# Kernel optimization log

Hardware: AMD Instinct MI355X
Metric: run time of the kernel (lower is better)

The kernel has to match this reference:

```python
import jax, jax.numpy as jnp
import numpy as np
from jax import lax

STRIDE, PAD, K = 1, 1, 3


def conv2d(x, w, b, stride, pad):
    y = lax.conv_general_dilated(x, w, (stride, stride), [(pad, pad), (pad, pad)],
                                 dimension_numbers=('NCHW', 'OIHW', 'NCHW'))
    return y + b[None, :, None, None]


def deform_conv2d(x, offset, mask, weight, stride, pad):
    # torchvision DeformConv2d v2 (modulated): offset channels are (dy, dx) pairs per tap.
    B, C, H, W = x.shape
    O = weight.shape[0]
    K2 = K * K
    Ho = (H + 2 * pad - K) // stride + 1
    Wo = (W + 2 * pad - K) // stride + 1
    off = offset.reshape(B, K2, 2, Ho, Wo)
    dy, dx = off[:, :, 0], off[:, :, 1]                      # [B,K2,Ho,Wo]
    ki = (jnp.arange(K2) // K).astype(x.dtype)[None, :, None, None]
    kj = (jnp.arange(K2) % K).astype(x.dtype)[None, :, None, None]
    hg = (jnp.arange(Ho) * stride - pad).astype(x.dtype)[None, None, :, None]
    wg = (jnp.arange(Wo) * stride - pad).astype(x.dtype)[None, None, None, :]
    py = hg + ki + dy                                        # sampling y coord [B,K2,Ho,Wo]
    px = wg + kj + dx
    y0 = jnp.floor(py)
    x0 = jnp.floor(px)
    ly = py - y0
    lx = px - x0
    y0i = y0.astype(jnp.int32)
    x0i = x0.astype(jnp.int32)
    x_flat = x.reshape(B, C, H * W)

    def gather(iy, ix):
        valid = ((iy >= 0) & (iy < H) & (ix >= 0) & (ix < W)).astype(x.dtype)
        idx = jnp.clip(iy, 0, H - 1) * W + jnp.clip(ix, 0, W - 1)   # [B,K2,Ho,Wo]
        v = jax.vmap(lambda xf, id_: xf[:, id_])(x_flat, idx)       # [B,C,K2,Ho,Wo]
        return v * valid[:, None]

    v = ((1 - ly) * (1 - lx))[:, None] * gather(y0i, x0i) \
      + ((1 - ly) * lx)[:, None] * gather(y0i, x0i + 1) \
      + (ly * (1 - lx))[:, None] * gather(y0i + 1, x0i) \
      + (ly * lx)[:, None] * gather(y0i + 1, x0i + 1)
    v = v * mask[:, None]                                    # modulate per tap
    return jnp.einsum('bckhw,ock->bohw', v, weight.reshape(O, C, K2))


def setup_inputs():
    key = jax.random.key(0)
    ks = jax.random.split(key, 5)
    B, C, H, W, O = 4, 64, 96, 96, 128
    x = jax.random.normal(ks[0], (B, C, H, W), jnp.float32)
    offset_w = jax.random.normal(ks[1], (2 * K * K, C, K, K), jnp.float32) * 0.01
    offset_b = jax.random.normal(ks[2], (2 * K * K,), jnp.float32) * 0.1
    mod_w = jax.random.normal(ks[3], (K * K, C, K, K), jnp.float32) * 0.01
    mod_b = jnp.zeros((K * K,), jnp.float32)
    deform_w = jax.random.normal(ks[4], (O, C, K, K), jnp.float32) * (1.0 / np.sqrt(C * K * K))
    return {"x": x, "offset_w": offset_w, "offset_b": offset_b,
            "mod_w": mod_w, "mod_b": mod_b, "deform_w": deform_w}


def reference(x, offset_w, offset_b, mod_w, mod_b, deform_w):
    offset = conv2d(x, offset_w, offset_b, STRIDE, PAD)
    modulator = 2.0 * jax.nn.sigmoid(conv2d(x, mod_w, mod_b, STRIDE, PAD))
    return deform_conv2d(x, offset, modulator, deform_w, STRIDE, PAD)
```

## Files before the change

kernel.cpp:

```cpp
#include <hip/hip_runtime.h>
#include <math.h>

#define Bc 4
#define Cc 64
#define Hh 96
#define Ww 96
#define Oo 128
#define HW 9216
#define PT 32
#define NPB 288
#define RR 7
#define RC 38
#define RS 72

typedef __attribute__((ext_vector_type(8))) short bf16x8;
typedef __attribute__((ext_vector_type(4))) float f32x4;
typedef __attribute__((ext_vector_type(4))) unsigned int u32x4;

__device__ inline float bf_lo(unsigned u) {
    return __builtin_bit_cast(float, u << 16);
}
__device__ inline float bf_hi(unsigned u) {
    return __builtin_bit_cast(float, u & 0xFFFF0000u);
}
__device__ inline unsigned cvt_pk_bf16(float lo, float hi) {
    unsigned r;
    asm("v_cvt_pk_bf16_f32 %0, %1, %2" : "=v"(r) : "v"(lo), "v"(hi));
    return r;
}

__global__ __launch_bounds__(256) void k_pre(
    const float* __restrict__ dw, const float* __restrict__ ow,
    const float* __restrict__ mw, const float* __restrict__ x,
    unsigned short* __restrict__ wTmF, unsigned short* __restrict__ w27F,
    unsigned short* __restrict__ xT)
{
    const int bid = blockIdx.x;
    const int t = threadIdx.x;
    if (bid < 180) {
        int i2 = (bid * 256 + t) * 2;
        if (i2 < 9 * 8 * 2 * 512) {
            int j = i2 & 7;
            int l = (i2 >> 3) & 63, fb = i2 >> 9;
            int s = fb & 1, m = (fb >> 1) & 7, k = fb >> 4;
            int oc = m * 16 + (l & 15);
            int c = s * 32 + (l >> 4) * 8 + j;
            float f0 = dw[(oc * 64 + c) * 9 + k];
            float f1 = dw[(oc * 64 + c + 1) * 9 + k];
            *(unsigned*)(wTmF + i2) = cvt_pk_bf16(f0, f1);
        } else {
            int jj = i2 - 9 * 8 * 2 * 512;
            if (jj < 9 * 2 * 2 * 512) {
                int j = jj & 7, l = (jj >> 3) & 63, fb2 = jj >> 9;
                int nt = fb2 & 1, s = (fb2 >> 1) & 1, k = fb2 >> 2;
                int ch = nt * 16 + (l & 15);
                int c = s * 32 + (l >> 4) * 8 + j;
                float f0 = 0.f, f1 = 0.f;
                if (ch < 18) {
                    f0 = ow[(ch * 64 + c) * 9 + k];
                    f1 = ow[(ch * 64 + c + 1) * 9 + k];
                } else if (ch < 27) {
                    f0 = mw[((ch - 18) * 64 + c) * 9 + k];
                    f1 = mw[((ch - 18) * 64 + c + 1) * 9 + k];
                }
                *(unsigned*)(w27F + jj) = cvt_pk_bf16(f0, f1);
            }
        }
    } else {
        int gp = (bid - 180) * 256 + t;
        int b = gp / HW;
        int p = gp - b * HW;
        const float* xb = x + (size_t)b * Cc * HW + p;
        unsigned short* op = xT + (size_t)gp * 64;
#pragma unroll
        for (int q = 0; q < 8; ++q) {
            union { bf16x8 v8; unsigned u[4]; } u;
#pragma unroll
            for (int c = 0; c < 8; c += 2) {
                float f0 = xb[(size_t)(q * 8 + c) * HW];
                float f1 = xb[(size_t)(q * 8 + c + 1) * HW];
                u.u[c >> 1] = cvt_pk_bf16(f0, f1);
            }
            *(bf16x8*)(op + q * 8) = u.v8;
        }
    }
}

template <int K0, int K1>
__device__ __forceinline__ void sample_gemm(
    const short (&reg)[RR * RC * RS],
    const unsigned short* __restrict__ xTb,
    const unsigned short* __restrict__ wb,
    const float (&pw)[9][4][PT], const int (&pi)[9][4][PT],
    int pos_l, int cq, f32x4 (&acc)[8])
{
#pragma unroll
    for (int kk = K0; kk < K1; ++kk) {
        const float w0 = pw[kk][0][pos_l], w1 = pw[kk][1][pos_l];
        const float w2 = pw[kk][2][pos_l], w3 = pw[kk][3][pos_l];
        const int i0 = pi[kk][0][pos_l], i1 = pi[kk][1][pos_l];
        const int i2 = pi[kk][2][pos_l], i3 = pi[kk][3][pos_l];
        const unsigned long long anybad = __ballot((i0 | i1 | i2 | i3) < 0);

#pragma unroll
        for (int s = 0; s < 2; ++s) {
            const int so = s * 32 + cq;
            bf16x8 c0, c1, c2, c3;
            if (anybad == 0) {
                c0 = *(const bf16x8*)(&reg[i0 + so]);
                c1 = *(const bf16x8*)(&reg[i1 + so]);
                c2 = *(const bf16x8*)(&reg[i2 + so]);
                c3 = *(const bf16x8*)(&reg[i3 + so]);
            } else {
                c0 = (i0 < 0) ? *(const bf16x8*)(xTb + (i0 & 0x7FFFFFFF) + so)
                              : *(const bf16x8*)(&reg[i0 + so]);
                c1 = (i1 < 0) ? *(const bf16x8*)(xTb + (i1 & 0x7FFFFFFF) + so)
                              : *(const bf16x8*)(&reg[i1 + so]);
                c2 = (i2 < 0) ? *(const bf16x8*)(xTb + (i2 & 0x7FFFFFFF) + so)
                              : *(const bf16x8*)(&reg[i2 + so]);
                c3 = (i3 < 0) ? *(const bf16x8*)(xTb + (i3 & 0x7FFFFFFF) + so)
                              : *(const bf16x8*)(&reg[i3 + so]);
            }
            const u32x4 U0 = __builtin_bit_cast(u32x4, c0);
            const u32x4 U1 = __builtin_bit_cast(u32x4, c1);
            const u32x4 U2 = __builtin_bit_cast(u32x4, c2);
            const u32x4 U3 = __builtin_bit_cast(u32x4, c3);
            union { bf16x8 v8; unsigned u[4]; } B;
#pragma unroll
            for (int p = 0; p < 4; ++p) {
                float r0 = w0 * bf_lo(U0[p]) + w1 * bf_lo(U1[p])
                         + w2 * bf_lo(U2[p]) + w3 * bf_lo(U3[p]);
                float r1 = w0 * bf_hi(U0[p]) + w1 * bf_hi(U1[p])
                         + w2 * bf_hi(U2[p]) + w3 * bf_hi(U3[p]);
                B.u[p] = cvt_pk_bf16(r0, r1);
            }
#pragma unroll
            for (int m = 0; m < 8; ++m) {
                bf16x8 A = *(const bf16x8*)(wb + (size_t)((kk * 16 + m * 2 + s) << 9));
                acc[m] = __builtin_amdgcn_mfma_f32_16x16x32_bf16(A, B.v8, acc[m], 0, 0, 0);
            }
        }
    }
}

__global__ __launch_bounds__(256, 3) void k_fused(
    const unsigned short* __restrict__ xT, const float* __restrict__ ob,
    const float* __restrict__ mb, const unsigned short* __restrict__ w27F,
    const unsigned short* __restrict__ wTmF, float* __restrict__ out)
{
    __shared__ union RU {
        short reg[RR * RC * RS];
        float mg[8 * 520];
    } R;
    __shared__ float s_pw[9][4][PT];
    __shared__ int   s_pi[9][4][PT];
    __shared__ float offm_s[27 * 33];

    const int t = threadIdx.x;
    const int lid = (blockIdx.x & 7) * 144 + (blockIdx.x >> 3);
    const int bb = lid / NPB;
    const int tile = lid - bb * NPB;
    const int ho = tile / 3;
    const int wo0 = (tile - ho * 3) * 32;
    const int wv = t >> 6;
    const int l = t & 63;
    const int lr = l & 15;
    const int quad = l >> 4;

    const unsigned short* xTb = xT + (size_t)bb * HW * 64;

    static const bf16x8 zero8 = {0, 0, 0, 0, 0, 0, 0, 0};
    for (int i = t; i < RR * RC * 8; i += 256) {
        int q = i & 7;
        int rcx = i >> 3;
        int col = rcx % RC, r = rcx / RC;
        int h = ho - 3 + r, w = wo0 - 3 + col;
        bf16x8 val = zero8;
        if ((unsigned)h < (unsigned)Hh && (unsigned)w < (unsigned)Ww)
            val = *(const bf16x8*)(xTb + ((size_t)(h * Ww + w)) * 64 + q * 8);
        *(bf16x8*)&R.reg[(r * RC + col) * RS + q * 8] = val;
    }
    __syncthreads();

    {
        f32x4 acc_o = {0.f, 0.f, 0.f, 0.f};
        const int mt1 = wv & 1;
        const int nt1 = wv >> 1;
#pragma unroll
        for (int k9 = 0; k9 < 9; ++k9) {
            const int di = k9 / 3, dj = k9 % 3;
            const short* ar =
                &R.reg[((di + 2) * RC + mt1 * 16 + lr + dj + 2) * RS + quad * 8];
#pragma unroll
            for (int s = 0; s < 2; ++s) {
                bf16x8 a = *(const bf16x8*)(ar + s * 32);
                bf16x8 b = *(const bf16x8*)(w27F + (((k9 * 2 + s) * 2 + nt1) << 9) + l * 8);
                acc_o = __builtin_amdgcn_mfma_f32_16x16x32_bf16(a, b, acc_o, 0, 0, 0);
            }
        }
        int ch = nt1 * 16 + lr;
        if (ch < 27) {
#pragma unroll
            for (int r = 0; r < 4; ++r)
                offm_s[ch * 33 + mt1 * 16 + quad * 4 + r] = acc_o[r];
        }
    }
    __syncthreads();

    for (int i = t; i < 27 * PT; i += 256) {
        int ch = i >> 5, pos = i & 31;
        float v = offm_s[ch * 33 + pos];
        if (ch < 18) v += ob[ch];
        else         v = 2.f / (1.f + expf(-(v + mb[ch - 18])));
        offm_s[ch * 33 + pos] = v;
    }
    __syncthreads();
    for (int i = t; i < 9 * PT; i += 256) {
        int kk = i >> 5, pos = i & 31;
        float dy = offm_s[(2 * kk) * 33 + pos];
        float dx = offm_s[(2 * kk + 1) * 33 + pos];
        float mm = offm_s[(18 + kk) * 33 + pos];
        float py = (float)(ho - 1 + kk / 3) + dy;
        float px = (float)(wo0 + pos - 1 + kk % 3) + dx;
        float fy = floorf(py), fx = floorf(px);
        float ly = py - fy, lx = px - fx;
        int y0 = (int)fy, x0 = (int)fx;
        int y1 = y0 + 1, x1 = x0 + 1;
        float v00 = ((unsigned)y0 < (unsigned)Hh && (unsigned)x0 < (unsigned)Ww) ? 1.f : 0.f;
        float v01 = ((unsigned)y0 < (unsigned)Hh && (unsigned)x1 < (unsigned)Ww) ? 1.f : 0.f;
        float v10 = ((unsigned)y1 < (unsigned)Hh && (unsigned)x0 < (unsigned)Ww) ? 1.f : 0.f;
        float v11 = ((unsigned)y1 < (unsigned)Hh && (unsigned)x1 < (unsigned)Ww) ? 1.f : 0.f;
        s_pw[kk][0][pos] = (1.f - ly) * (1.f - lx) * mm * v00;
        s_pw[kk][1][pos] = (1.f - ly) * lx * mm * v01;
        s_pw[kk][2][pos] = ly * (1.f - lx) * mm * v10;
        s_pw[kk][3][pos] = ly * lx * mm * v11;

        auto mkidx = [&](float valid, int y, int xx) -> int {
            if (valid == 0.f) return 0;
            int ry = y - (ho - 3), rx = xx - (wo0 - 3);
            if ((unsigned)ry < (unsigned)RR && (unsigned)rx < (unsigned)RC)
                return (ry * RC + rx) * RS;
            return (int)(0x80000000u | (unsigned)((y * Ww + xx) * 64));
        };
        s_pi[kk][0][pos] = mkidx(v00, y0, x0);
        s_pi[kk][1][pos] = mkidx(v01, y0, x1);
        s_pi[kk][2][pos] = mkidx(v10, y1, x0);
        s_pi[kk][3][pos] = mkidx(v11, y1, x1);
    }
    __syncthreads();

    const int nt = wv & 1;
    const int tg = wv >> 1;
    const int pos_l = nt * 16 + lr;
    const int cq = quad * 8;

    f32x4 acc[8];
#pragma unroll
    for (int m = 0; m < 8; ++m) acc[m] = (f32x4){0.f, 0.f, 0.f, 0.f};

    const unsigned short* wb = wTmF + l * 8;

    if (tg == 0)
        sample_gemm<0, 5>(R.reg, xTb, wb, s_pw, s_pi, pos_l, cq, acc);
    else
        sample_gemm<5, 9>(R.reg, xTb, wb, s_pw, s_pi, pos_l, cq, acc);

    __syncthreads();
    if (tg == 1) {
#pragma unroll
        for (int m = 0; m < 8; ++m)
            *(f32x4*)&R.mg[m * 520 + (nt * 64 + l) * 4] = acc[m];
    }
    __syncthreads();
    if (tg == 0) {
        float* outp = out + (size_t)bb * Oo * HW + tile * PT + nt * 16 + lr;
#pragma unroll
        for (int m = 0; m < 8; ++m) {
            f32x4 o = acc[m] + *(const f32x4*)&R.mg[m * 520 + (nt * 64 + l) * 4];
#pragma unroll
            for (int r = 0; r < 4; ++r) {
                int oc = m * 16 + quad * 4 + r;
                outp[(size_t)oc * HW] = o[r];
            }
        }
    }
}

extern "C" void kernel_launch(void* const* d_in, const int* in_sizes, int n_in,
                              void* d_out, int out_size, void* d_ws, size_t ws_size,
                              hipStream_t stream) {
    const float* x  = (const float*)d_in[0];
    const float* ow = (const float*)d_in[1];
    const float* ob = (const float*)d_in[2];
    const float* mw = (const float*)d_in[3];
    const float* mb = (const float*)d_in[4];
    const float* dw = (const float*)d_in[5];
    float* out = (float*)d_out;

    unsigned short* wTmF = (unsigned short*)d_ws;
    unsigned short* w27F = wTmF + 9 * 8 * 2 * 512;
    unsigned short* xT   = w27F + 9 * 2 * 2 * 512;

    hipLaunchKernelGGL(k_pre, dim3(324), dim3(256), 0, stream,
                       dw, ow, mw, x, wTmF, w27F, xT);
    hipLaunchKernelGGL(k_fused, dim3(Bc * NPB), dim3(256), 0, stream,
                       xT, ob, mb, w27F, wTmF, out);
}
```

Baseline: 108.2 us.

## Split deform sampling taps across eight waves with LDS tree reduction

Doubles the fused kernel block to 512 threads so four wave-groups each take 2-3 of the 9 kernel taps instead of two groups taking 4-5. Partial MFMA accumulators are combined through a two-stage LDS reduction before the output store. This shortens each wave's serial sampling and MFMA chain and raises wave count per CU. In exchange it adds extra barriers and LDS traffic, leaves half the waves idle in the offset conv, and drops full unrolling of the tap loop because the bounds are now runtime values.

```diff
diff --git a/kernel.cpp b/kernel.cpp
--- a/kernel.cpp
+++ b/kernel.cpp
@@ -86,16 +86,14 @@
     }
 }
 
-template <int K0, int K1>
 __device__ __forceinline__ void sample_gemm(
     const short (&reg)[RR * RC * RS],
     const unsigned short* __restrict__ xTb,
     const unsigned short* __restrict__ wb,
     const float (&pw)[9][4][PT], const int (&pi)[9][4][PT],
-    int pos_l, int cq, f32x4 (&acc)[8])
+    int pos_l, int cq, int k0, int k1, f32x4 (&acc)[8])
 {
-#pragma unroll
-    for (int kk = K0; kk < K1; ++kk) {
+    for (int kk = k0; kk < k1; ++kk) {
         const float w0 = pw[kk][0][pos_l], w1 = pw[kk][1][pos_l];
         const float w2 = pw[kk][2][pos_l], w3 = pw[kk][3][pos_l];
         const int i0 = pi[kk][0][pos_l], i1 = pi[kk][1][pos_l];
@@ -143,14 +141,14 @@
     }
 }
 
-__global__ __launch_bounds__(256, 3) void k_fused(
+__global__ __launch_bounds__(512, 4) void k_fused(
     const unsigned short* __restrict__ xT, const float* __restrict__ ob,
     const float* __restrict__ mb, const unsigned short* __restrict__ w27F,
     const unsigned short* __restrict__ wTmF, float* __restrict__ out)
 {
     __shared__ union RU {
         short reg[RR * RC * RS];
-        float mg[8 * 520];
+        float mg[2][8 * 128 * 4];
     } R;
     __shared__ float s_pw[9][4][PT];
     __shared__ int   s_pi[9][4][PT];
@@ -170,7 +168,7 @@
     const unsigned short* xTb = xT + (size_t)bb * HW * 64;
 
     static const bf16x8 zero8 = {0, 0, 0, 0, 0, 0, 0, 0};
-    for (int i = t; i < RR * RC * 8; i += 256) {
+    for (int i = t; i < RR * RC * 8; i += 512) {
         int q = i & 7;
         int rcx = i >> 3;
         int col = rcx % RC, r = rcx / RC;
@@ -182,7 +180,7 @@
     }
     __syncthreads();
 
-    {
+    if (wv < 4) {
         f32x4 acc_o = {0.f, 0.f, 0.f, 0.f};
         const int mt1 = wv & 1;
         const int nt1 = wv >> 1;
@@ -207,7 +205,7 @@
     }
     __syncthreads();
 
-    for (int i = t; i < 27 * PT; i += 256) {
+    for (int i = t; i < 27 * PT; i += 512) {
         int ch = i >> 5, pos = i & 31;
         float v = offm_s[ch * 33 + pos];
         if (ch < 18) v += ob[ch];
@@ -215,7 +213,7 @@
         offm_s[ch * 33 + pos] = v;
     }
     __syncthreads();
-    for (int i = t; i < 9 * PT; i += 256) {
+    for (int i = t; i < 9 * PT; i += 512) {
         int kk = i >> 5, pos = i & 31;
         float dy = offm_s[(2 * kk) * 33 + pos];
         float dx = offm_s[(2 * kk + 1) * 33 + pos];
@@ -253,6 +251,8 @@
     const int tg = wv >> 1;
     const int pos_l = nt * 16 + lr;
     const int cq = quad * 8;
+    const int k0 = (tg == 0) ? 0 : tg * 2 + 1;
+    const int k1 = k0 + ((tg == 0) ? 3 : 2);
 
     f32x4 acc[8];
 #pragma unroll
@@ -260,23 +260,37 @@
 
     const unsigned short* wb = wTmF + l * 8;
 
-    if (tg == 0)
-        sample_gemm<0, 5>(R.reg, xTb, wb, s_pw, s_pi, pos_l, cq, acc);
-    else
-        sample_gemm<5, 9>(R.reg, xTb, wb, s_pw, s_pi, pos_l, cq, acc);
-
+    sample_gemm(R.reg, xTb, wb, s_pw, s_pi, pos_l, cq, k0, k1, acc);
+
+    __syncthreads();
+
+    if (tg >= 2) {
+        float* mp = &R.mg[tg - 2][(nt * 64 + l) * 4];
+#pragma unroll
+        for (int m = 0; m < 8; ++m)
+            *(f32x4*)(mp + m * 128 * 4) = acc[m];
+    }
+    __syncthreads();
+    if (tg < 2) {
+        const float* mp = &R.mg[tg][(nt * 64 + l) * 4];
+#pragma unroll
+        for (int m = 0; m < 8; ++m)
+            acc[m] += *(const f32x4*)(mp + m * 128 * 4);
+    }
     __syncthreads();
     if (tg == 1) {
+        float* mp = &R.mg[0][(nt * 64 + l) * 4];
 #pragma unroll
         for (int m = 0; m < 8; ++m)
-            *(f32x4*)&R.mg[m * 520 + (nt * 64 + l) * 4] = acc[m];
+            *(f32x4*)(mp + m * 128 * 4) = acc[m];
     }
     __syncthreads();
     if (tg == 0) {
+        const float* mp = &R.mg[0][(nt * 64 + l) * 4];
         float* outp = out + (size_t)bb * Oo * HW + tile * PT + nt * 16 + lr;
 #pragma unroll
         for (int m = 0; m < 8; ++m) {
-            f32x4 o = acc[m] + *(const f32x4*)&R.mg[m * 520 + (nt * 64 + l) * 4];
+            f32x4 o = acc[m] + *(const f32x4*)(mp + m * 128 * 4);
 #pragma unroll
             for (int r = 0; r < 4; ++r) {
                 int oc = m * 16 + quad * 4 + r;
@@ -303,6 +317,6 @@
 
     hipLaunchKernelGGL(k_pre, dim3(324), dim3(256), 0, stream,
                        dw, ow, mw, x, wTmF, w27F, xT);
-    hipLaunchKernelGGL(k_fused, dim3(Bc * NPB), dim3(256), 0, stream,
+    hipLaunchKernelGGL(k_fused, dim3(Bc * NPB), dim3(512), 0, stream,
                        xT, ob, mb, w27F, wTmF, out);
 }
```

New measurement: 106.6 us. Within noise of the previous version (-1.4%).
